# Kernel optimization log

Hardware: AMD Instinct MI355X
Metric: run time of the kernel (lower is better)

The kernel has to match this reference:

```python
import jax, jax.numpy as jnp
import numpy as np
import math

B, S, D, L, FF = 16, 2048, 512, 4, 2048
VOCAB, ATTR_VOCAB, MAXPOS = 33, 608, 2048
EPS = 1e-5


def layernorm(x, w, b):
    mu = jnp.mean(x, axis=-1, keepdims=True)
    var = jnp.mean(jnp.square(x - mu), axis=-1, keepdims=True)
    return (x - mu) * jax.lax.rsqrt(var + EPS) * w + b


def setup_inputs() -> dict:
    key = jax.random.key(0)
    ks = jax.random.split(key, 16)
    std = 0.02
    return {
        "input_ids": jax.random.randint(ks[0], (B, S), 0, VOCAB),
        "combined_indices": jax.random.randint(ks[1], (B,), 0, ATTR_VOCAB),
        "attention_mask": jnp.ones((B, S), dtype=jnp.float32),
        "tok_emb": jax.random.normal(ks[2], (VOCAB, D), jnp.float32) * std,
        "pos_emb": jax.random.normal(ks[3], (MAXPOS, D), jnp.float32) * std,
        "attr_emb": jax.random.normal(ks[4], (ATTR_VOCAB, D), jnp.float32) * std,
        "ln_w": jnp.ones((L, D), jnp.float32),
        "ln_b": jnp.zeros((L, D), jnp.float32),
        "w1": jax.random.normal(ks[5], (L, D, FF), jnp.float32) * std,
        "b1": jnp.zeros((L, FF), jnp.float32),
        "w2": jax.random.normal(ks[6], (L, FF, D), jnp.float32) * std,
        "b2": jnp.zeros((L, D), jnp.float32),
        "out_w": jax.random.normal(ks[7], (D, VOCAB), jnp.float32) * std,
        "out_b": jnp.zeros((VOCAB,), jnp.float32),
    }


def reference(input_ids, combined_indices, attention_mask, tok_emb, pos_emb,
              attr_emb, ln_w, ln_b, w1, b1, w2, b2, out_w, out_b):
    scale = 1.0 / math.sqrt(D)
    # embeddings: token + position + per-example attribute (broadcast over seq)
    x = tok_emb[input_ids] + pos_emb[jnp.arange(S)][None, :, :] \
        + attr_emb[combined_indices][:, None, :]
    mask_add = (1.0 - attention_mask)[:, None, :] * -1e9  # [B,1,S]
    for l in range(L):
        h = layernorm(x, ln_w[l], ln_b[l])                 # shared LN params used twice
        scores = jnp.einsum('bsd,btd->bst', h, h) * scale + mask_add
        probs = jax.nn.softmax(scores, axis=-1)            # dropout=0 (eval)
        attn = jnp.einsum('bst,btd->bsd', probs, h) + x    # residual
        n2 = layernorm(attn, ln_w[l], ln_b[l])
        ff = jax.nn.gelu(n2 @ w1[l] + b1[l], approximate=False) @ w2[l] + b2[l]
        x = ff + attn
    return x @ out_w + out_b
```

## Files before the change

kernel.cpp:

```cpp
#include <hip/hip_runtime.h>
#include <hip/hip_bf16.h>
#include <cmath>

#define B_ 16
#define S_ 2048
#define D_ 512
#define L_ 4
#define FF_ 2048
#define V_ 33

typedef unsigned short u16;
typedef __attribute__((ext_vector_type(8))) short bf16x8;
typedef __attribute__((ext_vector_type(4))) float f32x4;

__device__ __forceinline__ u16 f2bf(float f) {
    unsigned x = __float_as_uint(f);
    unsigned r = (x + 0x7fffu + ((x >> 16) & 1u)) >> 16;
    return (u16)r;
}
__device__ __forceinline__ float bf2f(u16 u) { return __uint_as_float(((unsigned)u) << 16); }

__device__ __forceinline__ float wave_sum(float v) {
#pragma unroll
    for (int o = 32; o; o >>= 1) v += __shfl_xor(v, o);
    return v;
}

__device__ __forceinline__ void gload16(const u16* g, u16* l) {
    __builtin_amdgcn_global_load_lds((const __attribute__((address_space(1))) void*)g,
                                     (__attribute__((address_space(3))) void*)l, 16, 0, 0);
}

__device__ __forceinline__ uint4 pack8(const u16* ov) {
    uint4 p;
    p.x = (unsigned)ov[0] | ((unsigned)ov[1] << 16);
    p.y = (unsigned)ov[2] | ((unsigned)ov[3] << 16);
    p.z = (unsigned)ov[4] | ((unsigned)ov[5] << 16);
    p.w = (unsigned)ov[6] | ((unsigned)ov[7] << 16);
    return p;
}

__global__ __launch_bounds__(256) void embed_kernel(
    const int* __restrict__ ids, const int* __restrict__ attr,
    const float* __restrict__ tok, const float* __restrict__ pos,
    const float* __restrict__ attre, float* __restrict__ x)
{
    int idx = blockIdx.x * 256 + threadIdx.x;
    const int total = B_ * S_ * (D_ / 4);
    if (idx >= total) return;
    int d4 = idx & (D_ / 4 - 1);
    int bs = idx >> 7;
    int s  = bs & (S_ - 1);
    int b  = bs >> 11;
    int id = ids[bs];
    int a  = attr[b];
    float4 t  = ((const float4*)tok)[id * (D_ / 4) + d4];
    float4 p  = ((const float4*)pos)[s * (D_ / 4) + d4];
    float4 at = ((const float4*)attre)[a * (D_ / 4) + d4];
    float4 o;
    o.x = t.x + p.x + at.x; o.y = t.y + p.y + at.y;
    o.z = t.z + p.z + at.z; o.w = t.w + p.w + at.w;
    ((float4*)x)[idx] = o;
}

__global__ __launch_bounds__(256) void ln_kernel(
    const float* __restrict__ in, u16* __restrict__ out,
    const float* __restrict__ w, const float* __restrict__ b, int rows)
{
    int gw = (int)((blockIdx.x * 256 + threadIdx.x) >> 6);
    int lane = threadIdx.x & 63;
    if (gw >= rows) return;
    const float4* p = (const float4*)(in + (size_t)gw * D_);
    float4 a0 = p[lane * 2], a1 = p[lane * 2 + 1];
    float xv[8] = {a0.x, a0.y, a0.z, a0.w, a1.x, a1.y, a1.z, a1.w};
    float s = 0.f;
#pragma unroll
    for (int k = 0; k < 8; k++) s += xv[k];
    s = wave_sum(s);
    float mu = s * (1.f / D_);
    float q = 0.f;
#pragma unroll
    for (int k = 0; k < 8; k++) { float d = xv[k] - mu; q += d * d; }
    q = wave_sum(q);
    float rs = rsqrtf(q * (1.f / D_) + 1e-5f);
    const float4* w4 = (const float4*)w;
    const float4* b4 = (const float4*)b;
    float4 w0 = w4[lane * 2], w1v = w4[lane * 2 + 1];
    float4 b0 = b4[lane * 2], b1v = b4[lane * 2 + 1];
    float wv[8] = {w0.x, w0.y, w0.z, w0.w, w1v.x, w1v.y, w1v.z, w1v.w};
    float bv[8] = {b0.x, b0.y, b0.z, b0.w, b1v.x, b1v.y, b1v.z, b1v.w};
    u16 ov[8];
#pragma unroll
    for (int k = 0; k < 8; k++) ov[k] = f2bf((xv[k] - mu) * rs * wv[k] + bv[k]);
    *(uint4*)(out + (size_t)gw * D_ + lane * 8) = pack8(ov);
}

#define LTS 66
__global__ __launch_bounds__(1024) void lnT_kernel(
    const float* __restrict__ in, u16* __restrict__ h, u16* __restrict__ hT,
    const float* __restrict__ w, const float* __restrict__ b)
{
    __shared__ u16 tile[512 * LTS];
    const int tid = threadIdx.x, lane = tid & 63, wv = tid >> 6;
    const int rb = blockIdx.x;
    const int z  = rb >> 5;
    const int s0 = (rb & 31) * 64;

    float wv8[8], bv8[8];
#pragma unroll
    for (int k = 0; k < 8; k++) {
        wv8[k] = w[k * 64 + lane];
        bv8[k] = b[k * 64 + lane];
    }

#pragma unroll
    for (int i = 0; i < 4; i++) {
        const int rl = wv * 4 + i;
        const size_t grow = (size_t)rb * 64 + rl;
        const float* xr = in + grow * D_;
        float xv[8];
#pragma unroll
        for (int k = 0; k < 8; k++) xv[k] = xr[k * 64 + lane];
        float s = 0.f;
#pragma unroll
        for (int k = 0; k < 8; k++) s += xv[k];
        s = wave_sum(s);
        float mu = s * (1.f / D_);
        float q = 0.f;
#pragma unroll
        for (int k = 0; k < 8; k++) { float d = xv[k] - mu; q += d * d; }
        q = wave_sum(q);
        float rs = rsqrtf(q * (1.f / D_) + 1e-5f);
        u16* hr = h + grow * D_;
#pragma unroll
        for (int k = 0; k < 8; k++) {
            u16 v = f2bf((xv[k] - mu) * rs * wv8[k] + bv8[k]);
            hr[k * 64 + lane] = v;
            tile[(k * 64 + lane) * LTS + rl] = v;
        }
    }
    __syncthreads();
    u16* hb = hT + (size_t)z * S_ * D_;
#pragma unroll
    for (int it = 0; it < 4; it++) {
        int idx = it * 1024 + tid;
        int d = idx >> 3, sg = (idx & 7) << 3;
        u16 v[8];
#pragma unroll
        for (int i = 0; i < 8; i++) v[i] = tile[d * LTS + sg + i];
        *(uint4*)(hb + (size_t)d * S_ + s0 + sg) = pack8(v);
    }
}

__device__ __forceinline__ void ld2(const float* p, int idx, u16& a, u16& b) {
    float2 v = ((const float2*)p)[idx];
    a = f2bf(v.x); b = f2bf(v.y);
}
__device__ __forceinline__ void ld2(const u16* p, int idx, u16& a, u16& b) {
    unsigned v = ((const unsigned*)p)[idx];
    a = (u16)(v & 0xffff); b = (u16)(v >> 16);
}

template <typename T>
__global__ void transpose64(const T* __restrict__ in, u16* __restrict__ out,
                            int R, int C, size_t sIn, size_t sOut)
{
    __shared__ u16 tile[64][66];
    const T* ip = in + (size_t)blockIdx.z * sIn;
    u16* op = out + (size_t)blockIdx.z * sOut;
    const int tx = threadIdx.x, ty = threadIdx.y;
#pragma unroll
    for (int i = 0; i < 8; i++) {
        int r = blockIdx.y * 64 + ty + i * 8;
        u16 a, b;
        ld2(ip + (size_t)r * C, blockIdx.x * 32 + tx, a, b);
        tile[tx * 2 + 0][ty + i * 8] = a;
        tile[tx * 2 + 1][ty + i * 8] = b;
    }
    __syncthreads();
#pragma unroll
    for (int i = 0; i < 8; i++) {
        int ocl = ty + i * 8;
        int oc  = blockIdx.x * 64 + ocl;
        unsigned w = (unsigned)tile[ocl][tx * 2] | ((unsigned)tile[ocl][tx * 2 + 1] << 16);
        ((unsigned*)(op + (size_t)oc * R + blockIdx.y * 64))[tx] = w;
    }
}

enum { E_SC = 0, E_PV = 1, E_GELU = 2, E_FF2 = 3 };

template <int EPI>
__global__ __launch_bounds__(256) void gemm_nt(
    const u16* __restrict__ A, size_t sAz, int lda,
    const u16* __restrict__ B, size_t sBz, int ldb,
    float* Cf, u16* Cb, size_t sCz, int ldc,
    int K, float scale,
    const float* resid, size_t sRz,
    const float* __restrict__ bias,
    const float* __restrict__ aux, int b0,
    float* __restrict__ psum)
{
    __shared__ __align__(16) u16 ldsA[128 * 64];
    __shared__ __align__(16) u16 ldsB[128 * 64];
    __shared__ float l2[EPI == E_PV ? 128 : 1][2];

    const int gx = gridDim.x, gy = gridDim.y;
    const int nwg = gx * gy * gridDim.z;
    int lid = blockIdx.x + gx * (blockIdx.y + gy * blockIdx.z);
    {
        const int q = nwg >> 3, r = nwg & 7;
        const int xcd = lid & 7, idx = lid >> 3;
        lid = (xcd < r ? xcd * (q + 1) : r * (q + 1) + (xcd - r) * q) + idx;
    }
    const int bx = lid % gx;
    const int t2 = lid / gx;
    const int by = t2 % gy;
    const int z  = t2 / gy;

    A += (size_t)z * sAz;
    B += (size_t)z * sBz;
    const size_t coff = (size_t)z * sCz;
    const int brow = by * 128, bcol = bx * 128;
    const int tid = threadIdx.x, lane = tid & 63, wid = tid >> 6;
    const int wr = wid >> 1, wc = wid & 1;

    if constexpr (EPI == E_PV) {
        const int nrows = b0;
        const int base = z * S_ + brow;
        const int r = tid >> 1, ih = (tid & 1) << 4;
        float s = 0.f;
#pragma unroll
        for (int i = 0; i < 16; i++)
            s += aux[(size_t)(ih + i) * nrows + base + r];
        l2[r][tid & 1] = s;
    }

    f32x4 acc[4][4];
#pragma unroll
    for (int m = 0; m < 4; m++)
#pragma unroll
        for (int n = 0; n < 4; n++) acc[m][n] = 0.0f;

    const int lg   = lane >> 3;
    const int srow = wid * 8 + lg;
    const int skk  = ((lane & 7) ^ lg) << 3;

    const int l15 = lane & 15, l7 = lane & 7, kh = lane >> 4;

    for (int k0 = 0; k0 < K; k0 += 64) {
        __syncthreads();
#pragma unroll
        for (int r = 0; r < 4; r++) {
            const u16* ga = A + (size_t)(brow + r * 32 + srow) * lda + (k0 + skk);
            const u16* gb = B + (size_t)(bcol + r * 32 + srow) * ldb + (k0 + skk);
            gload16(ga, &ldsA[r * 2048 + wid * 512]);
            gload16(gb, &ldsB[r * 2048 + wid * 512]);
        }
        __syncthreads();
#pragma unroll
        for (int kk = 0; kk < 64; kk += 32) {
            const int kc = (kk >> 3) + kh;
            const int kswz = ((kc ^ l7) << 3);
            bf16x8 af[4], bfv[4];
#pragma unroll
            for (int m = 0; m < 4; m++)
                af[m] = *(const bf16x8*)&ldsA[(wr * 64 + m * 16 + l15) * 64 + kswz];
#pragma unroll
            for (int n = 0; n < 4; n++)
                bfv[n] = *(const bf16x8*)&ldsB[(wc * 64 + n * 16 + l15) * 64 + kswz];
#pragma unroll
            for (int m = 0; m < 4; m++)
#pragma unroll
                for (int n = 0; n < 4; n++)
                    acc[m][n] = __builtin_amdgcn_mfma_f32_16x16x32_bf16(af[m], bfv[n], acc[m][n], 0, 0, 0);
        }
    }

    float rsum[4][4];
#pragma unroll
    for (int m = 0; m < 4; m++)
#pragma unroll
        for (int j = 0; j < 4; j++) rsum[m][j] = 0.f;

#pragma unroll
    for (int m = 0; m < 4; m++)
#pragma unroll
        for (int n = 0; n < 4; n++) {
            int rowb = brow + wr * 64 + m * 16 + ((lane >> 4) << 2);
            int col  = bcol + wc * 64 + n * 16 + l15;
#pragma unroll
            for (int j = 0; j < 4; j++) {
                int row = rowb + j;
                float v = acc[m][n][j];
                size_t off = coff + (size_t)row * ldc + col;
                if constexpr (EPI == E_SC) {
                    float mv = aux[(size_t)(b0 + z) * S_ + col];
                    float ev = __expf(v * scale + (1.f - mv) * -1e9f);
                    Cb[off] = f2bf(ev);
                    rsum[m][j] += ev;
                } else if constexpr (EPI == E_PV) {
                    int rl = row - brow;
                    float lv = l2[rl][0] + l2[rl][1];
                    Cf[off] = v / lv + resid[(size_t)z * sRz + (size_t)row * ldc + col];
                } else if constexpr (EPI == E_GELU) {
                    float t = v + bias[col];
                    Cb[off] = f2bf(0.5f * t * (1.f + erff(t * 0.70710678118f)));
                } else {
                    Cf[off] = v + bias[col] + resid[(size_t)row * ldc + col];
                }
            }
        }

    if constexpr (EPI == E_SC) {
        const int nrows = gridDim.z * S_;
#pragma unroll
        for (int m = 0; m < 4; m++) {
            int rowl = brow + wr * 64 + m * 16 + ((lane >> 4) << 2);
#pragma unroll
            for (int j = 0; j < 4; j++) {
                float s = rsum[m][j];
                s += __shfl_xor(s, 1);
                s += __shfl_xor(s, 2);
                s += __shfl_xor(s, 4);
                s += __shfl_xor(s, 8);
                if (l15 == 0)
                    psum[(size_t)(bx * 2 + wc) * nrows + (size_t)z * S_ + rowl + j] = s;
            }
        }
    }
}

__global__ __launch_bounds__(256) void wtb_kernel(
    const float* __restrict__ W, u16* __restrict__ WTb)
{
    int i = blockIdx.x * 256 + threadIdx.x;
    if (i >= 64 * 512) return;
    int n = i >> 9, k = i & 511;
    WTb[i] = f2bf(n < V_ ? W[k * V_ + n] : 0.f);
}

__global__ __launch_bounds__(256) void outproj_mfma(
    const float* __restrict__ x, const u16* __restrict__ WTb,
    const float* __restrict__ bias, float* __restrict__ out)
{
    __shared__ __align__(16) u16 ldsA[128 * 64];
    __shared__ __align__(16) u16 ldsB[64 * 64];
    __shared__ float obuf[128][34];
    const int brow = blockIdx.x * 128;
    const int tid = threadIdx.x, lane = tid & 63, wid = tid >> 6;
    const int wr = wid >> 1, wc = wid & 1;
    const int l15 = lane & 15, l7 = lane & 7, kh = lane >> 4;
    const int lg = lane >> 3, srow = wid * 8 + lg;
    const int skk = ((lane & 7) ^ lg) << 3;
    const int ar = tid >> 1, ah = (tid & 1) * 32;

    f32x4 acc[4][2];
#pragma unroll
    for (int m = 0; m < 4; m++)
#pragma unroll
        for (int n = 0; n < 2; n++) acc[m][n] = 0.0f;

    for (int k0 = 0; k0 < 512; k0 += 64) {
        __syncthreads();
#pragma unroll
        for (int r = 0; r < 2; r++)
            gload16(WTb + (size_t)(r * 32 + srow) * 512 + (k0 + skk),
                    &ldsB[r * 2048 + wid * 512]);
        const float4* xs = (const float4*)(x + (size_t)(brow + ar) * 512 + k0 + ah);
#pragma unroll
        for (int j = 0; j < 4; j++) {
            float4 a = xs[j * 2], b = xs[j * 2 + 1];
            u16 t[8] = {f2bf(a.x), f2bf(a.y), f2bf(a.z), f2bf(a.w),
                        f2bf(b.x), f2bf(b.y), f2bf(b.z), f2bf(b.w)};
            int kc = (ah >> 3) + j;
            *(uint4*)&ldsA[ar * 64 + ((kc ^ (ar & 7)) << 3)] = pack8(t);
        }
        __syncthreads();
#pragma unroll
        for (int kk = 0; kk < 64; kk += 32) {
            const int kc = (kk >> 3) + kh;
            const int kswz = ((kc ^ l7) << 3);
            bf16x8 af[4], bfv[2];
#pragma unroll
            for (int m = 0; m < 4; m++)
                af[m] = *(const bf16x8*)&ldsA[(wr * 64 + m * 16 + l15) * 64 + kswz];
#pragma unroll
            for (int n = 0; n < 2; n++)
                bfv[n] = *(const bf16x8*)&ldsB[(wc * 32 + n * 16 + l15) * 64 + kswz];
#pragma unroll
            for (int m = 0; m < 4; m++)
#pragma unroll
                for (int n = 0; n < 2; n++)
                    acc[m][n] = __builtin_amdgcn_mfma_f32_16x16x32_bf16(af[m], bfv[n], acc[m][n], 0, 0, 0);
        }
    }

#pragma unroll
    for (int m = 0; m < 4; m++)
#pragma unroll
        for (int n = 0; n < 2; n++) {
            int rowl = wr * 64 + m * 16 + ((lane >> 4) << 2);
            int col  = wc * 32 + n * 16 + l15;
            if (col < V_) {
#pragma unroll
                for (int j = 0; j < 4; j++)
                    obuf[rowl + j][col] = acc[m][n][j] + bias[col];
            }
        }
    __syncthreads();
    float* ob = out + (size_t)brow * V_;
#pragma unroll 1
    for (int i = tid; i < 128 * V_; i += 256)
        ob[i] = obuf[i / V_][i % V_];
}

extern "C" void kernel_launch(void* const* d_in, const int* in_sizes, int n_in,
                              void* d_out, int out_size, void* d_ws, size_t ws_size,
                              hipStream_t stream)
{
    const int*   input_ids = (const int*)d_in[0];
    const int*   comb      = (const int*)d_in[1];
    const float* amask     = (const float*)d_in[2];
    const float* tok       = (const float*)d_in[3];
    const float* pos       = (const float*)d_in[4];
    const float* attre     = (const float*)d_in[5];
    const float* ln_w      = (const float*)d_in[6];
    const float* ln_b      = (const float*)d_in[7];
    const float* w1        = (const float*)d_in[8];
    const float* b1        = (const float*)d_in[9];
    const float* w2        = (const float*)d_in[10];
    const float* b2        = (const float*)d_in[11];
    const float* out_w     = (const float*)d_in[12];
    const float* out_b     = (const float*)d_in[13];
    float* out = (float*)d_out;
    (void)in_sizes; (void)n_in; (void)out_size;

    int NB_A, RC;
    if      (ws_size >= 335000000ULL) { NB_A = 16; RC = 32768; }
    else if (ws_size >= 215000000ULL) { NB_A = 8;  RC = 16384; }
    else if (ws_size >= 152000000ULL) { NB_A = 4;  RC = 8192;  }
    else                              { NB_A = 2;  RC = 4096;  }
    const int HR = NB_A * S_;

    unsigned char* ws = (unsigned char*)d_ws;
    size_t off = 0;
    auto carve = [&](size_t bytes) {
        void* p = ws + off;
        off += (bytes + 255) & ~(size_t)255;
        return p;
    };
    float* x    = (float*)carve((size_t)B_ * S_ * D_ * 4);
    u16* w1t    = (u16*)carve((size_t)L_ * D_ * FF_ * 2);
    u16* w2t    = (u16*)carve((size_t)L_ * D_ * FF_ * 2);
    u16* h      = (u16*)carve((size_t)HR * D_ * 2);
    u16* hT     = (u16*)carve((size_t)NB_A * S_ * D_ * 2);
    float* psum = (float*)carve((size_t)NB_A * S_ * 32 * 4);
    u16* WTb    = (u16*)carve((size_t)64 * 512 * 2);
    size_t scP_bytes  = (size_t)NB_A * S_ * S_ * 2;
    size_t tbuf_bytes = (size_t)RC * FF_ * 2;
    void* un = carve(scP_bytes > tbuf_bytes ? scP_bytes : tbuf_bytes);
    u16* scP  = (u16*)un;
    u16* tbuf = (u16*)un;

    const float scl = 1.0f / sqrtf((float)D_);
    const int nG = B_ / NB_A;
    const int nC = (B_ * S_) / RC;

    embed_kernel<<<(B_ * S_ * (D_ / 4)) / 256, 256, 0, stream>>>(input_ids, comb, tok, pos, attre, x);
    transpose64<float><<<dim3(FF_ / 64, D_ / 64, L_), dim3(32, 8), 0, stream>>>(
        w1, w1t, D_, FF_, (size_t)D_ * FF_, (size_t)FF_ * D_);
    transpose64<float><<<dim3(D_ / 64, FF_ / 64, L_), dim3(32, 8), 0, stream>>>(
        w2, w2t, FF_, D_, (size_t)FF_ * D_, (size_t)D_ * FF_);
    wtb_kernel<<<128, 256, 0, stream>>>(out_w, WTb);

    for (int l = 0; l < L_; l++) {
        const float* lw = ln_w + l * D_;
        const float* lb = ln_b + l * D_;

        for (int g = 0; g < nG; g++) {
            float* xg = x + (size_t)g * NB_A * S_ * D_;
            lnT_kernel<<<(NB_A * S_) / 64, 1024, 0, stream>>>(xg, h, hT, lw, lb);
            gemm_nt<E_SC><<<dim3(S_ / 128, S_ / 128, NB_A), 256, 0, stream>>>(
                h, (size_t)S_ * D_, D_,
                h, (size_t)S_ * D_, D_,
                nullptr, scP, (size_t)S_ * S_, S_,
                D_, scl, nullptr, 0, nullptr, amask, g * NB_A, psum);
            gemm_nt<E_PV><<<dim3(D_ / 128, S_ / 128, NB_A), 256, 0, stream>>>(
                scP, (size_t)S_ * S_, S_,
                hT, (size_t)S_ * D_, S_,
                xg, nullptr, (size_t)S_ * D_, D_,
                S_, 1.f, xg, (size_t)S_ * D_, nullptr, psum, NB_A * S_, nullptr);
        }

        for (int c = 0; c < nC; c++) {
            size_t roff = (size_t)c * RC;
            ln_kernel<<<RC / 4, 256, 0, stream>>>(x + roff * D_, h, lw, lb, RC);
            gemm_nt<E_GELU><<<dim3(FF_ / 128, RC / 128, 1), 256, 0, stream>>>(
                h, 0, D_,
                w1t + (size_t)l * FF_ * D_, 0, D_,
                nullptr, tbuf, 0, FF_,
                D_, 1.f, nullptr, 0, b1 + l * FF_, nullptr, 0, nullptr);
            gemm_nt<E_FF2><<<dim3(D_ / 128, RC / 128, 1), 256, 0, stream>>>(
                tbuf, 0, FF_,
                w2t + (size_t)l * D_ * FF_, 0, FF_,
                x + roff * D_, nullptr, 0, D_,
                FF_, 1.f, x + roff * D_, 0, b2 + l * D_, nullptr, 0, nullptr);
        }
    }

    outproj_mfma<<<(B_ * S_) / 128, 256, 0, stream>>>(x, WTb, out_b, out);
}
```

Baseline: 2.058 ms.

## Exploit symmetry of h·hᵀ scores by computing only upper-triangular tiles

The score matrix h·hᵀ is symmetric, so the new gemm_sc kernel launches only the 136 upper-triangular 128x128 tiles per batch instead of all 256. Each off-diagonal tile writes its exp'd scores and row partial sums, then recomputes exp with the row-side mask, transposes the result through LDS and writes the mirrored tile plus its column partial sums. This roughly halves the MFMA work of the score GEMM. In exchange it adds extra exp evaluations, an LDS transpose pass with synchronisation, and uneven per-block work (diagonal versus off-diagonal tiles).

```diff
diff --git a/kernel.cpp b/kernel.cpp
--- a/kernel.cpp
+++ b/kernel.cpp
@@ -187,7 +187,7 @@
     }
 }
 
-enum { E_SC = 0, E_PV = 1, E_GELU = 2, E_FF2 = 3 };
+enum { E_PV = 1, E_GELU = 2, E_FF2 = 3 };
 
 template <int EPI>
 __global__ __launch_bounds__(256) void gemm_nt(
@@ -197,8 +197,7 @@
     int K, float scale,
     const float* resid, size_t sRz,
     const float* __restrict__ bias,
-    const float* __restrict__ aux, int b0,
-    float* __restrict__ psum)
+    const float* __restrict__ aux, int b0)
 {
     __shared__ __align__(16) u16 ldsA[128 * 64];
     __shared__ __align__(16) u16 ldsB[128 * 64];
@@ -244,7 +243,6 @@
     const int lg   = lane >> 3;
     const int srow = wid * 8 + lg;
     const int skk  = ((lane & 7) ^ lg) << 3;
-
     const int l15 = lane & 15, l7 = lane & 7, kh = lane >> 4;
 
     for (int k0 = 0; k0 < K; k0 += 64) {
@@ -276,12 +274,6 @@
         }
     }
 
-    float rsum[4][4];
-#pragma unroll
-    for (int m = 0; m < 4; m++)
-#pragma unroll
-        for (int j = 0; j < 4; j++) rsum[m][j] = 0.f;
-
 #pragma unroll
     for (int m = 0; m < 4; m++)
 #pragma unroll
@@ -293,12 +285,7 @@
                 int row = rowb + j;
                 float v = acc[m][n][j];
                 size_t off = coff + (size_t)row * ldc + col;
-                if constexpr (EPI == E_SC) {
-                    float mv = aux[(size_t)(b0 + z) * S_ + col];
-                    float ev = __expf(v * scale + (1.f - mv) * -1e9f);
-                    Cb[off] = f2bf(ev);
-                    rsum[m][j] += ev;
-                } else if constexpr (EPI == E_PV) {
+                if constexpr (EPI == E_PV) {
                     int rl = row - brow;
                     float lv = l2[rl][0] + l2[rl][1];
                     Cf[off] = v / lv + resid[(size_t)z * sRz + (size_t)row * ldc + col];
@@ -310,21 +297,156 @@
                 }
             }
         }
-
-    if constexpr (EPI == E_SC) {
-        const int nrows = gridDim.z * S_;
-#pragma unroll
-        for (int m = 0; m < 4; m++) {
-            int rowl = brow + wr * 64 + m * 16 + ((lane >> 4) << 2);
+}
+
+__global__ __launch_bounds__(256) void gemm_sc(
+    const u16* __restrict__ h, u16* __restrict__ P,
+    const float* __restrict__ mask, int b0, float scale,
+    float* __restrict__ psum, int nbatch)
+{
+    __shared__ __align__(16) u16 ldsbuf[2][128 * 64];
+    u16* ldsA = ldsbuf[0];
+    u16* ldsB = ldsbuf[1];
+    u16* mt   = &ldsbuf[0][0];
+
+    const int nwg = 136 * nbatch;
+    int lid = blockIdx.x + 136 * blockIdx.z;
+    {
+        const int q = nwg >> 3, r = nwg & 7;
+        const int xcd = lid & 7, idx = lid >> 3;
+        lid = (xcd < r ? xcd * (q + 1) : r * (q + 1) + (xcd - r) * q) + idx;
+    }
+    int t = lid % 136;
+    const int z = lid / 136;
+    int by = 0;
+#pragma unroll 1
+    while (t >= 16 - by) { t -= 16 - by; by++; }
+    const int bx = by + t;
+
+    const u16* A = h + (size_t)z * S_ * D_;
+    const size_t coff = (size_t)z * S_ * S_;
+    const int brow = by * 128, bcol = bx * 128;
+    const int tid = threadIdx.x, lane = tid & 63, wid = tid >> 6;
+    const int wr = wid >> 1, wc = wid & 1;
+
+    f32x4 acc[4][4];
+#pragma unroll
+    for (int m = 0; m < 4; m++)
+#pragma unroll
+        for (int n = 0; n < 4; n++) acc[m][n] = 0.0f;
+
+    const int lg   = lane >> 3;
+    const int srow = wid * 8 + lg;
+    const int skk  = ((lane & 7) ^ lg) << 3;
+    const int l15 = lane & 15, l7 = lane & 7, kh = lane >> 4;
+
+    for (int k0 = 0; k0 < D_; k0 += 64) {
+        __syncthreads();
+#pragma unroll
+        for (int r = 0; r < 4; r++) {
+            const u16* ga = A + (size_t)(brow + r * 32 + srow) * D_ + (k0 + skk);
+            const u16* gb = A + (size_t)(bcol + r * 32 + srow) * D_ + (k0 + skk);
+            gload16(ga, &ldsA[r * 2048 + wid * 512]);
+            gload16(gb, &ldsB[r * 2048 + wid * 512]);
+        }
+        __syncthreads();
+#pragma unroll
+        for (int kk = 0; kk < 64; kk += 32) {
+            const int kc = (kk >> 3) + kh;
+            const int kswz = ((kc ^ l7) << 3);
+            bf16x8 af[4], bfv[4];
+#pragma unroll
+            for (int m = 0; m < 4; m++)
+                af[m] = *(const bf16x8*)&ldsA[(wr * 64 + m * 16 + l15) * 64 + kswz];
+#pragma unroll
+            for (int n = 0; n < 4; n++)
+                bfv[n] = *(const bf16x8*)&ldsB[(wc * 64 + n * 16 + l15) * 64 + kswz];
+#pragma unroll
+            for (int m = 0; m < 4; m++)
+#pragma unroll
+                for (int n = 0; n < 4; n++)
+                    acc[m][n] = __builtin_amdgcn_mfma_f32_16x16x32_bf16(af[m], bfv[n], acc[m][n], 0, 0, 0);
+        }
+    }
+
+    const float* mrow = mask + (size_t)(b0 + z) * S_;
+    const int nrows = nbatch * S_;
+
+    float rsum[4][4];
+#pragma unroll
+    for (int m = 0; m < 4; m++)
+#pragma unroll
+        for (int j = 0; j < 4; j++) rsum[m][j] = 0.f;
+
+#pragma unroll
+    for (int m = 0; m < 4; m++)
+#pragma unroll
+        for (int n = 0; n < 4; n++) {
+            int rowb = brow + wr * 64 + m * 16 + (kh << 2);
+            int col  = bcol + wc * 64 + n * 16 + l15;
+            float madd_c = (1.f - mrow[col]) * -1e9f;
 #pragma unroll
             for (int j = 0; j < 4; j++) {
-                float s = rsum[m][j];
-                s += __shfl_xor(s, 1);
-                s += __shfl_xor(s, 2);
-                s += __shfl_xor(s, 4);
-                s += __shfl_xor(s, 8);
-                if (l15 == 0)
-                    psum[(size_t)(bx * 2 + wc) * nrows + (size_t)z * S_ + rowl + j] = s;
+                int row = rowb + j;
+                float ev = __expf(acc[m][n][j] * scale + madd_c);
+                P[coff + (size_t)row * S_ + col] = f2bf(ev);
+                rsum[m][j] += ev;
+            }
+        }
+#pragma unroll
+    for (int m = 0; m < 4; m++) {
+        int rowl = brow + wr * 64 + m * 16 + (kh << 2);
+#pragma unroll
+        for (int j = 0; j < 4; j++) {
+            float s = rsum[m][j];
+            s += __shfl_xor(s, 1);
+            s += __shfl_xor(s, 2);
+            s += __shfl_xor(s, 4);
+            s += __shfl_xor(s, 8);
+            if (l15 == 0)
+                psum[(size_t)(bx * 2 + wc) * nrows + (size_t)z * S_ + rowl + j] = s;
+        }
+    }
+
+    if (bx != by) {
+#pragma unroll 1
+        for (int rnd = 0; rnd < 2; rnd++) {
+            __syncthreads();
+            if (wc == rnd) {
+#pragma unroll
+                for (int n = 0; n < 4; n++) {
+                    float csum = 0.f;
+                    const int mrow_l = n * 16 + l15;
+#pragma unroll
+                    for (int m = 0; m < 4; m++) {
+                        const int lr = wr * 64 + m * 16 + (kh << 2);
+                        u16 e2[4];
+#pragma unroll
+                        for (int j = 0; j < 4; j++) {
+                            float madd_r = (1.f - mrow[brow + lr + j]) * -1e9f;
+                            float em = __expf(acc[m][n][j] * scale + madd_r);
+                            csum += em;
+                            e2[j] = f2bf(em);
+                        }
+                        unsigned* m32 = (unsigned*)&mt[mrow_l * 136 + lr];
+                        m32[0] = (unsigned)e2[0] | ((unsigned)e2[1] << 16);
+                        m32[1] = (unsigned)e2[2] | ((unsigned)e2[3] << 16);
+                    }
+                    csum += __shfl_xor(csum, 16);
+                    csum += __shfl_xor(csum, 32);
+                    if (lane < 16)
+                        psum[(size_t)(by * 2 + wr) * nrows + (size_t)z * S_ +
+                             bcol + rnd * 64 + n * 16 + lane] = csum;
+                }
+            }
+            __syncthreads();
+#pragma unroll 1
+            for (int i = tid; i < 64 * 16; i += 256) {
+                int rr = i >> 4, c16 = (i & 15) << 3;
+                u16 v[8];
+#pragma unroll
+                for (int q = 0; q < 8; q++) v[q] = mt[rr * 136 + c16 + q];
+                *(uint4*)(P + coff + (size_t)(bcol + rnd * 64 + rr) * S_ + brow + c16) = pack8(v);
             }
         }
     }
@@ -480,16 +602,13 @@
         for (int g = 0; g < nG; g++) {
             float* xg = x + (size_t)g * NB_A * S_ * D_;
             lnT_kernel<<<(NB_A * S_) / 64, 1024, 0, stream>>>(xg, h, hT, lw, lb);
-            gemm_nt<E_SC><<<dim3(S_ / 128, S_ / 128, NB_A), 256, 0, stream>>>(
-                h, (size_t)S_ * D_, D_,
-                h, (size_t)S_ * D_, D_,
-                nullptr, scP, (size_t)S_ * S_, S_,
-                D_, scl, nullptr, 0, nullptr, amask, g * NB_A, psum);
+            gemm_sc<<<dim3(136, 1, NB_A), 256, 0, stream>>>(
+                h, scP, amask, g * NB_A, scl, psum, NB_A);
             gemm_nt<E_PV><<<dim3(D_ / 128, S_ / 128, NB_A), 256, 0, stream>>>(
                 scP, (size_t)S_ * S_, S_,
                 hT, (size_t)S_ * D_, S_,
                 xg, nullptr, (size_t)S_ * D_, D_,
-                S_, 1.f, xg, (size_t)S_ * D_, nullptr, psum, NB_A * S_, nullptr);
+                S_, 1.f, xg, (size_t)S_ * D_, nullptr, psum, NB_A * S_);
         }
 
         for (int c = 0; c < nC; c++) {
@@ -499,12 +618,12 @@
                 h, 0, D_,
                 w1t + (size_t)l * FF_ * D_, 0, D_,
                 nullptr, tbuf, 0, FF_,
-                D_, 1.f, nullptr, 0, b1 + l * FF_, nullptr, 0, nullptr);
+                D_, 1.f, nullptr, 0, b1 + l * FF_, nullptr, 0);
             gemm_nt<E_FF2><<<dim3(D_ / 128, RC / 128, 1), 256, 0, stream>>>(
                 tbuf, 0, FF_,
                 w2t + (size_t)l * D_ * FF_, 0, FF_,
                 x + roff * D_, nullptr, 0, D_,
-                FF_, 1.f, x + roff * D_, 0, b2 + l * D_, nullptr, 0, nullptr);
+                FF_, 1.f, x + roff * D_, 0, b2 + l * D_, nullptr, 0);
         }
     }
 
```

Result: faster. 2.005 ms (-2.6%).
